# Kernel tuning notes

Measured on AMD Instinct MI355X. Metric: run time of the kernel, lower is better.

The kernel has to match this reference:

```python
import jax, jax.numpy as jnp
import numpy as np

N = 20000      # nodes
E = 320000     # edges (avg degree 16)
DIN = 50       # PPI input features
C = 121        # PPI classes
HID = 1024     # 4 heads x 256 concatenated
H3 = 6         # heads in last layer


def setup_inputs() -> dict:
    key = jax.random.key(0)
    ks = jax.random.split(key, 7)
    X = jax.random.normal(ks[0], (N, DIN), jnp.float32)
    edge_index = jax.random.randint(ks[1], (2, E), 0, N, dtype=jnp.int32)
    def w(k, i, o):
        return jax.random.normal(k, (i, o), jnp.float32) / jnp.sqrt(jnp.float32(i))
    return {
        "X": X,
        "edge_index": edge_index,
        "W1": w(ks[2], DIN, HID),        # 4 heads x 256, concatenated
        "W2": w(ks[3], HID, HID),        # 4 heads x 256 GCN weights
        "S2": w(ks[4], HID, HID),        # 4 heads x 256 skip linears
        "W3": w(ks[5], HID, H3 * C),     # 6 heads x num_classes GCN weights
        "S3": w(ks[6], HID, H3 * C),     # 6 heads x num_classes skip linears
    }


def _agg(xw, row, col, norm, n):
    # GCN symmetric-normalized neighbor sum: out[col] += norm * xw[row]
    return jax.ops.segment_sum(xw[row] * norm[:, None], col, num_segments=n)


def reference(X, edge_index, W1, W2, S2, W3, S3):
    n = X.shape[0]
    row, col = edge_index[0], edge_index[1]
    # degree at targets (add_self_loops=False), D^{-1/2} A D^{-1/2} normalization
    deg = jax.ops.segment_sum(jnp.ones(row.shape, X.dtype), col, num_segments=n)
    dis = jnp.where(deg > 0, deg ** -0.5, 0.0)
    norm = dis[row] * dis[col]
    # layer 1: 4 GCN heads (weights concatenated), elu, concat
    h1 = jax.nn.elu(_agg(X @ W1, row, col, norm, n))              # [N, 1024]
    # layer 2: 4 GCN heads + linear skip, elu, concat
    h2 = jax.nn.elu(_agg(h1 @ W2, row, col, norm, n) + h1 @ S2)   # [N, 1024]
    # layer 3: 6 GCN heads + linear skip, average over heads (Identity act)
    y = _agg(h2 @ W3, row, col, norm, n) + h2 @ S3                # [N, 6*C]
    return y.reshape(n, H3, C).mean(axis=1)                       # [N, C]
```

## Files before the change

kernel.cpp:

```cpp
#include <hip/hip_runtime.h>
#include <hip/hip_bf16.h>
#include <math.h>

#define N_NODES 20000
#define N_EDGES 320000
#define DIN 50
#define HID 1024
#define NC3 726
#define NCLS 121
#define KCAT 2048
#define NQ 242

typedef __attribute__((ext_vector_type(8))) _Float16 half8;
typedef __attribute__((ext_vector_type(4))) float floatx4;

__device__ __forceinline__ unsigned short f2h(float v) {
    _Float16 h = (_Float16)v;
    return __builtin_bit_cast(unsigned short, h);
}
__device__ __forceinline__ float h2f(unsigned short u) {
    return (float)__builtin_bit_cast(_Float16, u);
}

__device__ __forceinline__ void async16(const void* g, void* l) {
    __builtin_amdgcn_global_load_lds(
        (const __attribute__((address_space(1))) void*)g,
        (__attribute__((address_space(3))) void*)l,
        16, 0, 0);
}


__global__ void zero_int_kernel(int* p, int n) {
    int i = blockIdx.x * blockDim.x + threadIdx.x;
    if (i < n) p[i] = 0;
}

__global__ __launch_bounds__(1024) void scan_kernel(const int* __restrict__ deg,
                                                    int* __restrict__ offs,
                                                    int* __restrict__ cursor,
                                                    float* __restrict__ dis,
                                                    int n, int total) {
    __shared__ int part[1024];
    int t = threadIdx.x;
    const int CH = (n + 1023) / 1024;
    int base0 = t * CH;
    int s = 0;
    for (int i = 0; i < CH; ++i) {
        int idx = base0 + i;
        if (idx < n) s += deg[idx];
    }
    part[t] = s;
    __syncthreads();
    for (int d = 1; d < 1024; d <<= 1) {
        int v = (t >= d) ? part[t - d] : 0;
        __syncthreads();
        part[t] += v;
        __syncthreads();
    }
    int run = part[t] - s;
    for (int i = 0; i < CH; ++i) {
        int idx = base0 + i;
        if (idx < n) {
            int d = deg[idx];
            offs[idx] = run;
            cursor[idx] = run;
            dis[idx] = d > 0 ? rsqrtf((float)d) : 0.0f;
            run += d;
        }
    }
    if (t == 1023) offs[n] = total;
}

__global__ void scatter_kernel(const int* __restrict__ row, const int* __restrict__ col,
                               const float* __restrict__ dis, int* __restrict__ cursor,
                               int* __restrict__ csr_src, float* __restrict__ csr_w, int e) {
    int i = blockIdx.x * blockDim.x + threadIdx.x;
    if (i < e) {
        int r = row[i], c = col[i];
        float nm = dis[r] * dis[c];
        int pos = atomicAdd(&cursor[c], 1);
        csr_src[pos] = r;
        csr_w[pos] = nm;
    }
}

__global__ __launch_bounds__(256) void prep_kernel(const int* __restrict__ ecol,
                                                   int* __restrict__ deg,
                                                   const float* __restrict__ W1,
                                                   unsigned short* __restrict__ Bt1,
                                                   const float* __restrict__ W2,
                                                   const float* __restrict__ S2,
                                                   unsigned short* __restrict__ Bt2,
                                                   const float* __restrict__ W3,
                                                   const float* __restrict__ S3,
                                                   unsigned short* __restrict__ Bt3) {
    __shared__ unsigned short tile[32][33];
    const int b = blockIdx.x;
    const int tid = threadIdx.x;

    if (b < 2048) {
        int src = b >> 10;
        int t = b & 1023;
        int k0 = (t >> 5) * 32;
        int n0 = (t & 31) * 32;
        const float* W = src ? S2 : W2;
        int koff = src ? HID : 0;
        int tx = tid & 31;
        int ty = tid >> 5;
#pragma unroll
        for (int r = 0; r < 32; r += 8)
            tile[ty + r][tx] = f2h(W[(size_t)(k0 + ty + r) * HID + n0 + tx]);
        __syncthreads();
#pragma unroll
        for (int r = 0; r < 32; r += 8)
            Bt2[(size_t)(n0 + ty + r) * KCAT + koff + k0 + tx] = tile[tx][ty + r];
    } else if (b < 2304) {
        int tb = b - 2048;
        int src = tb >> 7;
        int t = tb & 127;
        int k0 = (t >> 2) * 32;
        int c0 = (t & 3) * 32;
        const float* W = src ? S3 : W3;
        int tx = tid & 31;
        int ty = tid >> 5;
#pragma unroll
        for (int r = 0; r < 32; r += 8) {
            int k = k0 + ty + r, c = c0 + tx;
            float v = 0.0f;
            if (c < NCLS) {
                const float* p = W + (size_t)k * NC3 + c;
                v = (p[0] + p[121] + p[242] + p[363] + p[484] + p[605]) * (1.0f / 6.0f);
            }
            tile[ty + r][tx] = f2h(v);
        }
        __syncthreads();
#pragma unroll
        for (int r = 0; r < 32; r += 8) {
            int c = c0 + ty + r;
            if (c < NCLS)
                Bt3[(size_t)(src * NCLS + c) * HID + k0 + tx] = tile[tx][ty + r];
        }
    } else if (b < 2560) {
        int i = (b - 2304) * 256 + tid;
        int n = i / 64, k = i - n * 64;
        Bt1[i] = (k < DIN) ? f2h(W1[(size_t)k * HID + n]) : (unsigned short)0;
    } else {
        int i = (b - 2560) * 256 + tid;
        if (i < N_EDGES) atomicAdd(&deg[ecol[i]], 1);
    }
}


__global__ __launch_bounds__(64) void aggX_kernel(const float* __restrict__ X,
                                                  const int* __restrict__ offs,
                                                  const int* __restrict__ csr_src,
                                                  const float* __restrict__ csr_w,
                                                  unsigned short* __restrict__ gX) {
    int n = blockIdx.x;
    int t = threadIdx.x;
    float a = 0.0f;
    if (t < DIN) {
        int p0 = offs[n], p1 = offs[n + 1];
        for (int p = p0; p < p1; ++p) {
            a = fmaf(csr_w[p], X[(size_t)csr_src[p] * DIN + t], a);
        }
    }
    gX[(size_t)n * 64 + t] = (t < DIN) ? f2h(a) : (unsigned short)0;
}

__global__ __launch_bounds__(256) void agg_slice_kernel(const unsigned short* __restrict__ h,
                                                        const int* __restrict__ offs,
                                                        const int* __restrict__ csr_src,
                                                        const float* __restrict__ csr_w,
                                                        unsigned short* __restrict__ g) {
    const int f = blockIdx.x;
    const int slice = f & 7;
    const int nb = f >> 3;
    const int tid = threadIdx.x;
    const int n = nb * 16 + (tid >> 4);
    const int coloff = slice * 128 + (tid & 15) * 8;
    const unsigned short* hp = h + coloff;

    float a[8] = {0, 0, 0, 0, 0, 0, 0, 0};
    int p0 = offs[n], p1 = offs[n + 1];
    for (int p = p0; p < p1; ++p) {
        int s = csr_src[p];
        float w = csr_w[p];
        uint4 v = *(const uint4*)&hp[(size_t)s * HID];
        const unsigned short* vs = (const unsigned short*)&v;
#pragma unroll
        for (int j = 0; j < 8; ++j) a[j] = fmaf(w, h2f(vs[j]), a[j]);
    }
    unsigned short ov[8];
#pragma unroll
    for (int j = 0; j < 8; ++j) ov[j] = f2h(a[j]);
    *(uint4*)&g[(size_t)n * HID + coloff] = *(const uint4*)ov;
}

__global__ __launch_bounds__(256) void agg3_kernel(const unsigned short* __restrict__ Q,
                                                   const int* __restrict__ offs,
                                                   const int* __restrict__ csr_src,
                                                   const float* __restrict__ csr_w,
                                                   float* __restrict__ out) {
    int n = blockIdx.x * 2 + (threadIdx.x >> 7);
    int c = threadIdx.x & 127;
    if (c >= NCLS) return;
    float a = 0.0f;
    int p0 = offs[n], p1 = offs[n + 1];
    for (int p = p0; p < p1; ++p) {
        a = fmaf(csr_w[p], h2f(Q[(size_t)csr_src[p] * NQ + c]), a);
    }
    a += h2f(Q[(size_t)n * NQ + NCLS + c]);
    out[(size_t)n * NCLS + c] = a;
}


#define GBM 128
#define GBN 128
#define GBK 32
#define MII 4

template <int EPI>
__global__ __launch_bounds__(256, 4) void mfma_gemm_kernel(
        const unsigned short* __restrict__ Ag, const unsigned short* __restrict__ Ah,
        const unsigned short* __restrict__ Bt,
        void* __restrict__ Co,
        int M, int N, int ldc, int ktot, int khalf, int kw,
        int NB, int MB, int mchunk) {
    __shared__ __align__(16) unsigned short sA[2][GBM * GBK];
    __shared__ __align__(16) unsigned short sB[2][GBN * GBK];

    const int f = blockIdx.x;
    const int xcd = f & 7;
    const int r0 = f >> 3;
    const int grp = r0 / (NB * MII);
    const int rem = r0 % (NB * MII);
    const int nB = rem / MII;
    const int mi = grp * MII + rem % MII;
    const int mB = xcd * mchunk + mi;
    if (mB >= MB) return;
    const int bm = mB * GBM;
    const int bn = nB * GBN;
    const int ks = blockIdx.y;

    const int tid = threadIdx.x;
    const int lane = tid & 63;
    const int wave = tid >> 6;
    const int wm = wave >> 1;
    const int wn = wave & 1;

    const int st_r = tid >> 2;
    const int st_slot = tid & 3;
    const int st_c = (st_slot ^ ((st_r >> 1) & 3)) * 8;
    const int st_lds = st_r * GBK + st_slot * 8;

    int agm[2], bgn[2];
#pragma unroll
    for (int p = 0; p < 2; ++p) {
        int gm = bm + st_r + p * 64;
        agm[p] = gm < M ? gm : M - 1;
        int gn = bn + st_r + p * 64;
        bgn[p] = gn < N ? gn : N - 1;
    }

    const int frow = lane & 15;
    const int fkc = (((lane >> 4) ^ ((frow >> 1) & 3))) * 8;

    floatx4 acc[4][4];
#pragma unroll
    for (int i = 0; i < 4; ++i)
#pragma unroll
        for (int j = 0; j < 4; ++j) acc[i][j] = (floatx4){0.f, 0.f, 0.f, 0.f};

    auto issue = [&](int k0, int buf) {
        const unsigned short* ap = (k0 < khalf) ? Ag : Ah;
        int ka = (k0 < khalf) ? k0 : k0 - khalf;
#pragma unroll
        for (int p = 0; p < 2; ++p) {
            async16(&ap[(size_t)agm[p] * khalf + ka + st_c],
                    &sA[buf][p * 64 * GBK + st_lds]);
            async16(&Bt[(size_t)bgn[p] * ktot + k0 + st_c],
                    &sB[buf][p * 64 * GBK + st_lds]);
        }
    };

    const int tw = kw / GBK;
    const int t0 = ks * tw;
    const int t1 = t0 + tw;

    issue(t0 * GBK, 0);

    for (int t = t0; t < t1; ++t) {
        __syncthreads();
        if (t + 1 < t1) issue((t + 1) * GBK, (t + 1) & 1);

        const unsigned short* a_base = sA[t & 1];
        const unsigned short* b_base = sB[t & 1];
        half8 fa[4], fb[4];
#pragma unroll
        for (int i = 0; i < 4; ++i)
            fa[i] = *(const half8*)&a_base[(wm * 64 + i * 16 + frow) * GBK + fkc];
#pragma unroll
        for (int j = 0; j < 4; ++j)
            fb[j] = *(const half8*)&b_base[(wn * 64 + j * 16 + frow) * GBK + fkc];
#pragma unroll
        for (int i = 0; i < 4; ++i)
#pragma unroll
            for (int j = 0; j < 4; ++j)
                acc[i][j] = __builtin_amdgcn_mfma_f32_16x16x32_f16(fa[i], fb[j], acc[i][j], 0, 0, 0);
    }

    const int c_r0 = (lane >> 4) * 4;
    const int c_c = lane & 15;
#pragma unroll
    for (int i = 0; i < 4; ++i)
#pragma unroll
        for (int j = 0; j < 4; ++j) {
            int gn = bn + wn * 64 + j * 16 + c_c;
            if (gn >= N) continue;
#pragma unroll
            for (int r = 0; r < 4; ++r) {
                int gm = bm + wm * 64 + i * 16 + c_r0 + r;
                if (gm >= M) continue;
                float v = acc[i][j][r];
                if (EPI == 0) {
                    v = v > 0 ? v : expf(v) - 1.0f;
                    ((unsigned short*)Co)[(size_t)gm * ldc + gn] = f2h(v);
                } else if (EPI == 1) {
                    atomicAdd(&((float*)Co)[(size_t)gm * ldc + gn], v);
                } else {
                    ((unsigned short*)Co)[(size_t)gm * ldc + gn] = f2h(v);
                }
            }
        }
}


static inline size_t align_up(size_t x, size_t a) { return (x + a - 1) & ~(a - 1); }

extern "C" void kernel_launch(void* const* d_in, const int* in_sizes, int n_in,
                              void* d_out, int out_size, void* d_ws, size_t ws_size,
                              hipStream_t stream) {
    const float* X  = (const float*)d_in[0];
    const int* erow = (const int*)d_in[1];
    const int* ecol = (const int*)d_in[1] + N_EDGES;
    const float* W1 = (const float*)d_in[2];
    const float* W2 = (const float*)d_in[3];
    const float* S2 = (const float*)d_in[4];
    const float* W3 = (const float*)d_in[5];
    const float* S3 = (const float*)d_in[6];
    float* out = (float*)d_out;

    char* w = (char*)d_ws;
    int* deg     = (int*)w;             w += align_up((size_t)N_NODES * 4, 256);
    int* offs    = (int*)w;             w += align_up((size_t)(N_NODES + 1) * 4, 256);
    int* cursor  = (int*)w;             w += align_up((size_t)N_NODES * 4, 256);
    int* csr_src = (int*)w;             w += align_up((size_t)N_EDGES * 4, 256);
    float* dis   = (float*)w;           w += align_up((size_t)N_NODES * 4, 256);
    float* csr_w = (float*)w;           w += align_up((size_t)N_EDGES * 4, 256);
    unsigned short* gXh = (unsigned short*)w; w += align_up((size_t)N_NODES * 64 * 2, 256);
    unsigned short* h1 = (unsigned short*)w;  w += align_up((size_t)N_NODES * HID * 2, 256);
    unsigned short* g  = (unsigned short*)w;  w += align_up((size_t)N_NODES * HID * 2, 256);
    unsigned short* h2 = (unsigned short*)w;  w += align_up((size_t)N_NODES * HID * 2, 256);
    unsigned short* Qh = (unsigned short*)w;  w += align_up((size_t)N_NODES * NQ * 2, 256);
    unsigned short* Bt1 = (unsigned short*)w; w += align_up((size_t)HID * 64 * 2, 256);
    unsigned short* Bt2 = (unsigned short*)w; w += align_up((size_t)HID * KCAT * 2, 256);
    unsigned short* Bt3 = (unsigned short*)w; w += align_up((size_t)NQ * HID * 2, 256);

    const int TB = 256;
    int nb_n = (N_NODES + TB - 1) / TB;

    zero_int_kernel<<<nb_n, TB, 0, stream>>>(deg, N_NODES);
    prep_kernel<<<3810, 256, 0, stream>>>(ecol, deg, W1, Bt1, W2, S2, Bt2, W3, S3, Bt3);

    scan_kernel<<<1, 1024, 0, stream>>>(deg, offs, cursor, dis, N_NODES, N_EDGES);
    scatter_kernel<<<(N_EDGES + TB - 1) / TB, TB, 0, stream>>>(erow, ecol, dis, cursor,
                                                               csr_src, csr_w, N_EDGES);

    const int MB = (N_NODES + GBM - 1) / GBM;
    const int mchunk = (MB + 7) / 8;
    const int NB2 = HID / GBN;
    const int NB3 = (NQ + GBN - 1) / GBN;
    const int AGG_GRID = 8 * (N_NODES / 16);

    aggX_kernel<<<N_NODES, 64, 0, stream>>>(X, offs, csr_src, csr_w, gXh);
    mfma_gemm_kernel<0><<<dim3(8 * mchunk * NB2, 1), 256, 0, stream>>>(
        gXh, gXh, Bt1, h1, N_NODES, HID, HID, 64, 64, 64, NB2, MB, mchunk);

    agg_slice_kernel<<<AGG_GRID, 256, 0, stream>>>(h1, offs, csr_src, csr_w, g);
    mfma_gemm_kernel<0><<<dim3(8 * mchunk * NB2, 1), 256, 0, stream>>>(
        g, h1, Bt2, h2, N_NODES, HID, HID, KCAT, HID, KCAT, NB2, MB, mchunk);

    mfma_gemm_kernel<2><<<dim3(8 * mchunk * NB3, 1), 256, 0, stream>>>(
        h2, h2, Bt3, Qh, N_NODES, NQ, NQ, HID, HID, HID, NB3, MB, mchunk);
    agg3_kernel<<<N_NODES / 2, 256, 0, stream>>>(Qh, offs, csr_src, csr_w, out);
}
```

Before: 489.4 us.

## Split-K layer-3 GEMM into fp32 buffer, reshape aggregation slices, simplify GEMM block order

The layer-3 GEMM is split along K into two halves that accumulate (EPI=1, presumably atomically) into a new fp32 Q buffer, which is zero-filled by extra blocks appended to the prep kernel. agg3 now reads that fp32 buffer instead of fp16. The layer-2 aggregation uses 64-column slices with 32 nodes per block and maps slices to XCDs. The GEMM tile order drops the MII grouping in favour of a plain row-major mapping. The aims are more parallelism in the narrow layer-3 GEMM and better L2 locality in the gather, at the cost of atomics, a zero-fill pass and twice the Q traffic.

Measured after the change: 534.9 us. 9.3% more time.

```diff
diff --git a/kernel.cpp b/kernel.cpp
--- a/kernel.cpp
+++ b/kernel.cpp
@@ -84,6 +84,10 @@
     }
 }
 
+#define NQF (N_NODES * NQ)
+#define NQF4 (NQF / 4)
+#define NZQ4 ((NQF4 + 255) / 256)
+
 __global__ __launch_bounds__(256) void prep_kernel(const int* __restrict__ ecol,
                                                    int* __restrict__ deg,
                                                    const float* __restrict__ W1,
@@ -93,7 +97,8 @@
                                                    unsigned short* __restrict__ Bt2,
                                                    const float* __restrict__ W3,
                                                    const float* __restrict__ S3,
-                                                   unsigned short* __restrict__ Bt3) {
+                                                   unsigned short* __restrict__ Bt3,
+                                                   float* __restrict__ Qf) {
     __shared__ unsigned short tile[32][33];
     const int b = blockIdx.x;
     const int tid = threadIdx.x;
@@ -144,9 +149,12 @@
         int i = (b - 2304) * 256 + tid;
         int n = i / 64, k = i - n * 64;
         Bt1[i] = (k < DIN) ? f2h(W1[(size_t)k * HID + n]) : (unsigned short)0;
-    } else {
+    } else if (b < 3810) {
         int i = (b - 2560) * 256 + tid;
         if (i < N_EDGES) atomicAdd(&deg[ecol[i]], 1);
+    } else {
+        int i4 = (b - 3810) * 256 + tid;
+        if (i4 < NQF4) ((float4*)Qf)[i4] = (float4){0.f, 0.f, 0.f, 0.f};
     }
 }
 
@@ -174,11 +182,14 @@
                                                         const float* __restrict__ csr_w,
                                                         unsigned short* __restrict__ g) {
     const int f = blockIdx.x;
-    const int slice = f & 7;
-    const int nb = f >> 3;
+    const int xcd = f & 7;
+    const int r0 = f >> 3;
+    const int s_outer = r0 / 625;
+    const int nb = r0 % 625;
+    const int slice = s_outer * 8 + xcd;
     const int tid = threadIdx.x;
-    const int n = nb * 16 + (tid >> 4);
-    const int coloff = slice * 128 + (tid & 15) * 8;
+    const int n = nb * 32 + (tid >> 3);
+    const int coloff = slice * 64 + (tid & 7) * 8;
     const unsigned short* hp = h + coloff;
 
     float a[8] = {0, 0, 0, 0, 0, 0, 0, 0};
@@ -197,7 +208,7 @@
     *(uint4*)&g[(size_t)n * HID + coloff] = *(const uint4*)ov;
 }
 
-__global__ __launch_bounds__(256) void agg3_kernel(const unsigned short* __restrict__ Q,
+__global__ __launch_bounds__(256) void agg3_kernel(const float* __restrict__ Qf,
                                                    const int* __restrict__ offs,
                                                    const int* __restrict__ csr_src,
                                                    const float* __restrict__ csr_w,
@@ -208,9 +219,9 @@
     float a = 0.0f;
     int p0 = offs[n], p1 = offs[n + 1];
     for (int p = p0; p < p1; ++p) {
-        a = fmaf(csr_w[p], h2f(Q[(size_t)csr_src[p] * NQ + c]), a);
-    }
-    a += h2f(Q[(size_t)n * NQ + NCLS + c]);
+        a = fmaf(csr_w[p], Qf[(size_t)csr_src[p] * NQ + c], a);
+    }
+    a += Qf[(size_t)n * NQ + NCLS + c];
     out[(size_t)n * NCLS + c] = a;
 }
 
@@ -218,7 +229,6 @@
 #define GBM 128
 #define GBN 128
 #define GBK 32
-#define MII 4
 
 template <int EPI>
 __global__ __launch_bounds__(256, 4) void mfma_gemm_kernel(
@@ -233,10 +243,8 @@
     const int f = blockIdx.x;
     const int xcd = f & 7;
     const int r0 = f >> 3;
-    const int grp = r0 / (NB * MII);
-    const int rem = r0 % (NB * MII);
-    const int nB = rem / MII;
-    const int mi = grp * MII + rem % MII;
+    const int nB = r0 % NB;
+    const int mi = r0 / NB;
     const int mB = xcd * mchunk + mi;
     if (mB >= MB) return;
     const int bm = mB * GBM;
@@ -358,11 +366,11 @@
     int* csr_src = (int*)w;             w += align_up((size_t)N_EDGES * 4, 256);
     float* dis   = (float*)w;           w += align_up((size_t)N_NODES * 4, 256);
     float* csr_w = (float*)w;           w += align_up((size_t)N_EDGES * 4, 256);
+    float* Qf    = (float*)w;           w += align_up((size_t)NQF * 4, 256);
     unsigned short* gXh = (unsigned short*)w; w += align_up((size_t)N_NODES * 64 * 2, 256);
     unsigned short* h1 = (unsigned short*)w;  w += align_up((size_t)N_NODES * HID * 2, 256);
     unsigned short* g  = (unsigned short*)w;  w += align_up((size_t)N_NODES * HID * 2, 256);
     unsigned short* h2 = (unsigned short*)w;  w += align_up((size_t)N_NODES * HID * 2, 256);
-    unsigned short* Qh = (unsigned short*)w;  w += align_up((size_t)N_NODES * NQ * 2, 256);
     unsigned short* Bt1 = (unsigned short*)w; w += align_up((size_t)HID * 64 * 2, 256);
     unsigned short* Bt2 = (unsigned short*)w; w += align_up((size_t)HID * KCAT * 2, 256);
     unsigned short* Bt3 = (unsigned short*)w; w += align_up((size_t)NQ * HID * 2, 256);
@@ -371,7 +379,8 @@
     int nb_n = (N_NODES + TB - 1) / TB;
 
     zero_int_kernel<<<nb_n, TB, 0, stream>>>(deg, N_NODES);
-    prep_kernel<<<3810, 256, 0, stream>>>(ecol, deg, W1, Bt1, W2, S2, Bt2, W3, S3, Bt3);
+    prep_kernel<<<3810 + NZQ4, 256, 0, stream>>>(ecol, deg, W1, Bt1, W2, S2, Bt2,
+                                                 W3, S3, Bt3, Qf);
 
     scan_kernel<<<1, 1024, 0, stream>>>(deg, offs, cursor, dis, N_NODES, N_EDGES);
     scatter_kernel<<<(N_EDGES + TB - 1) / TB, TB, 0, stream>>>(erow, ecol, dis, cursor,
@@ -381,7 +390,7 @@
     const int mchunk = (MB + 7) / 8;
     const int NB2 = HID / GBN;
     const int NB3 = (NQ + GBN - 1) / GBN;
-    const int AGG_GRID = 8 * (N_NODES / 16);
+    const int AGG_GRID = 8 * 1250;
 
     aggX_kernel<<<N_NODES, 64, 0, stream>>>(X, offs, csr_src, csr_w, gXh);
     mfma_gemm_kernel<0><<<dim3(8 * mchunk * NB2, 1), 256, 0, stream>>>(
@@ -391,7 +400,7 @@
     mfma_gemm_kernel<0><<<dim3(8 * mchunk * NB2, 1), 256, 0, stream>>>(
         g, h1, Bt2, h2, N_NODES, HID, HID, KCAT, HID, KCAT, NB2, MB, mchunk);
 
-    mfma_gemm_kernel<2><<<dim3(8 * mchunk * NB3, 1), 256, 0, stream>>>(
-        h2, h2, Bt3, Qh, N_NODES, NQ, NQ, HID, HID, HID, NB3, MB, mchunk);
-    agg3_kernel<<<N_NODES / 2, 256, 0, stream>>>(Qh, offs, csr_src, csr_w, out);
-}
+    mfma_gemm_kernel<1><<<dim3(8 * mchunk * NB3, 2), 256, 0, stream>>>(
+        h2, h2, Bt3, Qf, N_NODES, NQ, NQ, HID, HID, HID / 2, NB3, MB, mchunk);
+    agg3_kernel<<<N_NODES / 2, 256, 0, stream>>>(Qf, offs, csr_src, csr_w, out);
+}
```
